# Kernel optimization log

Measured on AMD Instinct MI355X. Metric: run time of the kernel, lower is better.

## Reference

```python
import jax, jax.numpy as jnp
import numpy as np

B, S, D, E, F = 2, 2048, 1024, 8, 4096


def setup_inputs() -> dict:
    key = jax.random.key(0)
    k1, k2, k3, k4 = jax.random.split(key, 4)
    x = jax.random.normal(k1, (B, S, D), dtype=jnp.float32)
    gate_w = jax.random.normal(k2, (E, D), dtype=jnp.float32) * 0.02
    w1 = jax.random.normal(k3, (E, D, F), dtype=jnp.float32) * 0.02
    w2 = jax.random.normal(k4, (E, F, D), dtype=jnp.float32) * 0.02
    return {"x": x, "gate_w": gate_w, "w1": w1, "w2": w2}


def reference(x, gate_w, w1, w2):
    b, s, d = x.shape
    n_experts = w1.shape[0]
    tokens = x.reshape(-1, d)                      # (T, D)
    logits = tokens @ gate_w.T                     # (T, E) router (Linear, no bias)
    expert_ids = jnp.argmax(logits, axis=-1)       # top-1 routing (T,)
    dispatch = jax.nn.one_hot(expert_ids, n_experts, dtype=tokens.dtype)  # (T, E)
    # dense all-experts reference of the grouped GEMM: h_e = tokens @ w1[e]
    h = jnp.einsum('td,edf->etf', tokens, w1)      # (E, T, F)
    h = jax.nn.gelu(h, approximate=False)          # torch F.gelu default = exact erf
    out_e = jnp.einsum('etf,efd->etd', h, w2)      # (E, T, D)
    # scatter back: each token takes exactly its assigned expert's output
    out = jnp.einsum('etd,te->td', out_e, dispatch)
    return out.reshape(b, s, d)
```

## Files before the change

kernel.cpp:

```cpp
#include <hip/hip_runtime.h>
#include <hip/hip_bf16.h>
#include <math.h>

#define T_TOK 4096
#define D_DIM 1024
#define E_EXP 8
#define F_DIM 4096
#define BM 128
#define BN 128
#define BK 32
#define LDK 40
#define MAX_TILES 40

typedef __attribute__((ext_vector_type(8))) short short8;
typedef __attribute__((ext_vector_type(4))) float float4v;

__device__ __forceinline__ short f2b(float f) {
    union { float f; unsigned u; } v; v.f = f;
    unsigned r = v.u + 0x7fffu + ((v.u >> 16) & 1u);
    return (short)(r >> 16);
}

__global__ void router_kernel(const float* __restrict__ x, const float* __restrict__ gw,
                              int* __restrict__ eid, int* __restrict__ rnk,
                              int* __restrict__ counts) {
    int lane = threadIdx.x & 63;
    int wave = threadIdx.x >> 6;
    int t = blockIdx.x * 4 + wave;
    const float* xr = x + (size_t)t * D_DIM;
    float p[E_EXP];
#pragma unroll
    for (int e = 0; e < E_EXP; ++e) p[e] = 0.f;
#pragma unroll
    for (int i = 0; i < D_DIM / 64; ++i) {
        float v = xr[lane + 64 * i];
#pragma unroll
        for (int e = 0; e < E_EXP; ++e)
            p[e] = fmaf(v, gw[e * D_DIM + lane + 64 * i], p[e]);
    }
#pragma unroll
    for (int off = 32; off > 0; off >>= 1) {
#pragma unroll
        for (int e = 0; e < E_EXP; ++e) p[e] += __shfl_down(p[e], off, 64);
    }
    if (lane == 0) {
        int best = 0; float bv = p[0];
#pragma unroll
        for (int e = 1; e < E_EXP; ++e) if (p[e] > bv) { bv = p[e]; best = e; }
        eid[t] = best;
        rnk[t] = atomicAdd(&counts[best], 1);
    }
}

__global__ void prefix_kernel(const int* __restrict__ counts, int* __restrict__ offsets,
                              int* __restrict__ tmap) {
    int off = 0;
    offsets[0] = 0;
    int nt = 0;
    for (int e = 0; e < E_EXP; ++e) {
        int c = counts[e];
        for (int m0 = 0; m0 < c; m0 += BM) {
            tmap[nt * 3 + 0] = e;
            tmap[nt * 3 + 1] = off + m0;
            tmap[nt * 3 + 2] = (c - m0 < BM) ? (c - m0) : BM;
            ++nt;
        }
        off += c;
        offsets[e + 1] = off;
    }
    for (; nt < MAX_TILES; ++nt) tmap[nt * 3 + 2] = 0;
}

__global__ void scatter_kernel(const int* __restrict__ eid, const int* __restrict__ rnk,
                               const int* __restrict__ offsets, int* __restrict__ sorted) {
    int t = blockIdx.x * 256 + threadIdx.x;
    sorted[offsets[eid[t]] + rnk[t]] = t;
}

__global__ __launch_bounds__(256) void gemm1_kernel(const float* __restrict__ x,
                                                    const float* __restrict__ w1,
                                                    const int* __restrict__ sorted,
                                                    const int* __restrict__ tmap,
                                                    short* __restrict__ hbuf) {
    __shared__ short As[BM * LDK];
    __shared__ short Bs[BN * LDK];
    __shared__ int srow[BM];
    int mt = blockIdx.y;
    int m_count = tmap[mt * 3 + 2];
    if (m_count == 0) return;
    int e = tmap[mt * 3 + 0];
    int row0 = tmap[mt * 3 + 1];
    int n0 = blockIdx.x * BN;
    int tid = threadIdx.x;
    if (tid < BM) srow[tid] = sorted[row0 + (tid < m_count ? tid : m_count - 1)];
    __syncthreads();

    int lane = tid & 63, wave = tid >> 6;
    int wm = (wave & 1) * 64, wn = (wave >> 1) * 64;
    float4v acc[4][4];
#pragma unroll
    for (int i = 0; i < 4; ++i)
#pragma unroll
        for (int j = 0; j < 4; ++j) acc[i][j] = (float4v)(0.f);

    int ar = tid >> 1;
    int ac = (tid & 1) * 16;
    int bn = tid & 127;
    int bq = (tid >> 7) * 16;
    const float* abase = x + (size_t)srow[ar] * D_DIM + ac;
    const float* bbase = w1 + (size_t)e * D_DIM * F_DIM + (size_t)bq * F_DIM + (n0 + bn);

    for (int k0 = 0; k0 < D_DIM; k0 += BK) {
        {
            const float* ap = abase + k0;
            float4v f0 = *(const float4v*)(ap);
            float4v f1 = *(const float4v*)(ap + 4);
            float4v f2 = *(const float4v*)(ap + 8);
            float4v f3 = *(const float4v*)(ap + 12);
            short8 s0, s1;
#pragma unroll
            for (int c = 0; c < 4; ++c) {
                s0[c] = f2b(f0[c]); s0[4 + c] = f2b(f1[c]);
                s1[c] = f2b(f2[c]); s1[4 + c] = f2b(f3[c]);
            }
            *(short8*)(&As[ar * LDK + ac]) = s0;
            *(short8*)(&As[ar * LDK + ac + 8]) = s1;
        }
        {
            const float* bp = bbase + (size_t)k0 * F_DIM;
            float v[16];
#pragma unroll
            for (int j = 0; j < 16; ++j) v[j] = bp[(size_t)j * F_DIM];
            short8 s0, s1;
#pragma unroll
            for (int j = 0; j < 8; ++j) { s0[j] = f2b(v[j]); s1[j] = f2b(v[8 + j]); }
            *(short8*)(&Bs[bn * LDK + bq]) = s0;
            *(short8*)(&Bs[bn * LDK + bq + 8]) = s1;
        }
        __syncthreads();
        short8 af[4], bf[4];
#pragma unroll
        for (int i = 0; i < 4; ++i)
            af[i] = *(const short8*)(&As[(wm + i * 16 + (lane & 15)) * LDK + (lane >> 4) * 8]);
#pragma unroll
        for (int j = 0; j < 4; ++j)
            bf[j] = *(const short8*)(&Bs[(wn + j * 16 + (lane & 15)) * LDK + (lane >> 4) * 8]);
#pragma unroll
        for (int i = 0; i < 4; ++i)
#pragma unroll
            for (int j = 0; j < 4; ++j)
                acc[i][j] = __builtin_amdgcn_mfma_f32_16x16x32_bf16(af[i], bf[j], acc[i][j], 0, 0, 0);
        __syncthreads();
    }
    int rbase = (lane >> 4) * 4;
    int cbase = lane & 15;
#pragma unroll
    for (int i = 0; i < 4; ++i) {
#pragma unroll
        for (int r = 0; r < 4; ++r) {
            int row = wm + i * 16 + rbase + r;
            if (row < m_count) {
                short* hp = hbuf + (size_t)(row0 + row) * F_DIM + n0 + wn + cbase;
#pragma unroll
                for (int j = 0; j < 4; ++j) {
                    float s = acc[i][j][r];
                    float g = 0.5f * s * (1.f + erff(s * 0.70710678118f));
                    hp[j * 16] = f2b(g);
                }
            }
        }
    }
}

__global__ __launch_bounds__(256) void gemm2_kernel(const short* __restrict__ hbuf,
                                                    const float* __restrict__ w2,
                                                    const int* __restrict__ sorted,
                                                    const int* __restrict__ tmap,
                                                    float* __restrict__ out) {
    __shared__ short As[BM * LDK];
    __shared__ short Bs[BN * LDK];
    __shared__ int srow[BM];
    int mt = blockIdx.y;
    int m_count = tmap[mt * 3 + 2];
    if (m_count == 0) return;
    int e = tmap[mt * 3 + 0];
    int row0 = tmap[mt * 3 + 1];
    int n0 = blockIdx.x * BN;
    int tid = threadIdx.x;
    if (tid < BM) srow[tid] = sorted[row0 + (tid < m_count ? tid : m_count - 1)];
    __syncthreads();

    int lane = tid & 63, wave = tid >> 6;
    int wm = (wave & 1) * 64, wn = (wave >> 1) * 64;
    float4v acc[4][4];
#pragma unroll
    for (int i = 0; i < 4; ++i)
#pragma unroll
        for (int j = 0; j < 4; ++j) acc[i][j] = (float4v)(0.f);

    int ar = tid >> 1;
    int ac = (tid & 1) * 16;
    int bn = tid & 127;
    int bq = (tid >> 7) * 16;
    int arc = ar < m_count ? ar : m_count - 1;
    const short* abase = hbuf + (size_t)(row0 + arc) * F_DIM + ac;
    const float* bbase = w2 + (size_t)e * F_DIM * D_DIM + (size_t)bq * D_DIM + (n0 + bn);

    for (int k0 = 0; k0 < F_DIM; k0 += BK) {
        {
            const short* ap = abase + k0;
            *(short8*)(&As[ar * LDK + ac]) = *(const short8*)(ap);
            *(short8*)(&As[ar * LDK + ac + 8]) = *(const short8*)(ap + 8);
        }
        {
            const float* bp = bbase + (size_t)k0 * D_DIM;
            float v[16];
#pragma unroll
            for (int j = 0; j < 16; ++j) v[j] = bp[(size_t)j * D_DIM];
            short8 s0, s1;
#pragma unroll
            for (int j = 0; j < 8; ++j) { s0[j] = f2b(v[j]); s1[j] = f2b(v[8 + j]); }
            *(short8*)(&Bs[bn * LDK + bq]) = s0;
            *(short8*)(&Bs[bn * LDK + bq + 8]) = s1;
        }
        __syncthreads();
        short8 af[4], bf[4];
#pragma unroll
        for (int i = 0; i < 4; ++i)
            af[i] = *(const short8*)(&As[(wm + i * 16 + (lane & 15)) * LDK + (lane >> 4) * 8]);
#pragma unroll
        for (int j = 0; j < 4; ++j)
            bf[j] = *(const short8*)(&Bs[(wn + j * 16 + (lane & 15)) * LDK + (lane >> 4) * 8]);
#pragma unroll
        for (int i = 0; i < 4; ++i)
#pragma unroll
            for (int j = 0; j < 4; ++j)
                acc[i][j] = __builtin_amdgcn_mfma_f32_16x16x32_bf16(af[i], bf[j], acc[i][j], 0, 0, 0);
        __syncthreads();
    }
    int rbase = (lane >> 4) * 4;
    int cbase = lane & 15;
#pragma unroll
    for (int i = 0; i < 4; ++i) {
#pragma unroll
        for (int r = 0; r < 4; ++r) {
            int row = wm + i * 16 + rbase + r;
            if (row < m_count) {
                float* op = out + (size_t)srow[row] * D_DIM + n0 + wn + cbase;
#pragma unroll
                for (int j = 0; j < 4; ++j) op[j * 16] = acc[i][j][r];
            }
        }
    }
}

extern "C" void kernel_launch(void* const* d_in, const int* in_sizes, int n_in,
                              void* d_out, int out_size, void* d_ws, size_t ws_size,
                              hipStream_t stream) {
    const float* x  = (const float*)d_in[0];
    const float* gw = (const float*)d_in[1];
    const float* w1 = (const float*)d_in[2];
    const float* w2 = (const float*)d_in[3];
    float* out = (float*)d_out;
    char* ws = (char*)d_ws;

    int* counts  = (int*)(ws);
    int* offsets = (int*)(ws + 64);
    int* tmap    = (int*)(ws + 128);
    int* eid     = (int*)(ws + 1024);
    int* rnk     = (int*)(ws + 17408);
    int* sorted  = (int*)(ws + 33792);
    short* hbuf  = (short*)(ws + 51200);

    hipMemsetAsync(counts, 0, 32, stream);
    router_kernel<<<T_TOK / 4, 256, 0, stream>>>(x, gw, eid, rnk, counts);
    prefix_kernel<<<1, 1, 0, stream>>>(counts, offsets, tmap);
    scatter_kernel<<<T_TOK / 256, 256, 0, stream>>>(eid, rnk, offsets, sorted);
    gemm1_kernel<<<dim3(F_DIM / BN, MAX_TILES), 256, 0, stream>>>(x, w1, sorted, tmap, hbuf);
    gemm2_kernel<<<dim3(D_DIM / BN, MAX_TILES), 256, 0, stream>>>(hbuf, w2, sorted, tmap, out);
}
```

Baseline: 555.4 us.

## Pre-convert inputs and transposed weights to bf16, split-K gemm2 with atomics

Adds kernels that convert x to bf16 and transpose-convert w1/w2 into K-contiguous bf16 layouts in workspace, so the GEMMs can load operands with plain vector loads instead of converting fp32 inside the main loop. gemm2 is split along F into four K-slices that accumulate into a zeroed output with atomicAdd, raising the number of blocks. The weight conversion runs on every call and moves all 256MB of fp32 weights, which may outweigh the savings. Atomics also make the fp32 summation order nondeterministic.

```diff
diff --git a/kernel.cpp b/kernel.cpp
--- a/kernel.cpp
+++ b/kernel.cpp
@@ -1,5 +1,4 @@
 #include <hip/hip_runtime.h>
-#include <hip/hip_bf16.h>
 #include <math.h>
 
 #define T_TOK 4096
@@ -11,6 +10,7 @@
 #define BK 32
 #define LDK 40
 #define MAX_TILES 40
+#define KSPLIT 4
 
 typedef __attribute__((ext_vector_type(8))) short short8;
 typedef __attribute__((ext_vector_type(4))) float float4v;
@@ -75,6 +75,189 @@
                                const int* __restrict__ offsets, int* __restrict__ sorted) {
     int t = blockIdx.x * 256 + threadIdx.x;
     sorted[offsets[eid[t]] + rnk[t]] = t;
+}
+
+__global__ __launch_bounds__(256) void cvt_x_kernel(const float* __restrict__ x,
+                                                    short* __restrict__ xb) {
+    size_t base = ((size_t)blockIdx.x * 256 + threadIdx.x) * 16;
+    float4v f0 = *(const float4v*)(x + base);
+    float4v f1 = *(const float4v*)(x + base + 4);
+    float4v f2 = *(const float4v*)(x + base + 8);
+    float4v f3 = *(const float4v*)(x + base + 12);
+    short8 s0, s1;
+#pragma unroll
+    for (int c = 0; c < 4; ++c) {
+        s0[c] = f2b(f0[c]); s0[4 + c] = f2b(f1[c]);
+        s1[c] = f2b(f2[c]); s1[4 + c] = f2b(f3[c]);
+    }
+    *(short8*)(xb + base) = s0;
+    *(short8*)(xb + base + 8) = s1;
+}
+
+__global__ __launch_bounds__(256) void tconv_kernel(const float* __restrict__ in,
+                                                    short* __restrict__ outp, int R, int C) {
+    __shared__ short t[64][72];
+    size_t slab = (size_t)R * C;
+    const float* ip = in + (size_t)blockIdx.z * slab + (size_t)(blockIdx.y * 64) * C + blockIdx.x * 64;
+    short* op = outp + (size_t)blockIdx.z * slab + (size_t)(blockIdx.x * 64) * R + blockIdx.y * 64;
+    int tid = threadIdx.x;
+    int r = tid >> 2, c4 = (tid & 3) * 16;
+    const float* p = ip + (size_t)r * C + c4;
+    float4v f0 = *(const float4v*)(p);
+    float4v f1 = *(const float4v*)(p + 4);
+    float4v f2 = *(const float4v*)(p + 8);
+    float4v f3 = *(const float4v*)(p + 12);
+#pragma unroll
+    for (int j = 0; j < 4; ++j) {
+        t[c4 + j][r]      = f2b(f0[j]);
+        t[c4 + 4 + j][r]  = f2b(f1[j]);
+        t[c4 + 8 + j][r]  = f2b(f2[j]);
+        t[c4 + 12 + j][r] = f2b(f3[j]);
+    }
+    __syncthreads();
+    short* q = op + (size_t)r * R + c4;
+    *(short8*)q       = *(const short8*)&t[r][c4];
+    *(short8*)(q + 8) = *(const short8*)&t[r][c4 + 8];
+}
+
+__global__ __launch_bounds__(256) void gemm1_bf16(const short* __restrict__ xb,
+                                                  const short* __restrict__ w1b,
+                                                  const int* __restrict__ sorted,
+                                                  const int* __restrict__ tmap,
+                                                  short* __restrict__ hbuf) {
+    __shared__ short As[BM * LDK];
+    __shared__ short Bs[BN * LDK];
+    __shared__ int srow[BM];
+    int mt = blockIdx.y;
+    int m_count = tmap[mt * 3 + 2];
+    if (m_count == 0) return;
+    int e = tmap[mt * 3 + 0];
+    int row0 = tmap[mt * 3 + 1];
+    int n0 = blockIdx.x * BN;
+    int tid = threadIdx.x;
+    if (tid < BM) srow[tid] = sorted[row0 + (tid < m_count ? tid : m_count - 1)];
+    __syncthreads();
+
+    int lane = tid & 63, wave = tid >> 6;
+    int wm = (wave & 1) * 64, wn = (wave >> 1) * 64;
+    float4v acc[4][4];
+#pragma unroll
+    for (int i = 0; i < 4; ++i)
+#pragma unroll
+        for (int j = 0; j < 4; ++j) acc[i][j] = (float4v)(0.f);
+
+    int r2 = tid >> 1;
+    int c2 = (tid & 1) * 16;
+    const short* abase = xb + (size_t)srow[r2] * D_DIM + c2;
+    const short* bbase = w1b + (size_t)e * D_DIM * F_DIM + (size_t)(n0 + r2) * D_DIM + c2;
+
+    for (int k0 = 0; k0 < D_DIM; k0 += BK) {
+        *(short8*)(&As[r2 * LDK + c2])     = *(const short8*)(abase + k0);
+        *(short8*)(&As[r2 * LDK + c2 + 8]) = *(const short8*)(abase + k0 + 8);
+        *(short8*)(&Bs[r2 * LDK + c2])     = *(const short8*)(bbase + k0);
+        *(short8*)(&Bs[r2 * LDK + c2 + 8]) = *(const short8*)(bbase + k0 + 8);
+        __syncthreads();
+        short8 af[4], bf[4];
+#pragma unroll
+        for (int i = 0; i < 4; ++i)
+            af[i] = *(const short8*)(&As[(wm + i * 16 + (lane & 15)) * LDK + (lane >> 4) * 8]);
+#pragma unroll
+        for (int j = 0; j < 4; ++j)
+            bf[j] = *(const short8*)(&Bs[(wn + j * 16 + (lane & 15)) * LDK + (lane >> 4) * 8]);
+#pragma unroll
+        for (int i = 0; i < 4; ++i)
+#pragma unroll
+            for (int j = 0; j < 4; ++j)
+                acc[i][j] = __builtin_amdgcn_mfma_f32_16x16x32_bf16(af[i], bf[j], acc[i][j], 0, 0, 0);
+        __syncthreads();
+    }
+    int rbase = (lane >> 4) * 4;
+    int cbase = lane & 15;
+#pragma unroll
+    for (int i = 0; i < 4; ++i) {
+#pragma unroll
+        for (int r = 0; r < 4; ++r) {
+            int row = wm + i * 16 + rbase + r;
+            if (row < m_count) {
+                short* hp = hbuf + (size_t)(row0 + row) * F_DIM + n0 + wn + cbase;
+#pragma unroll
+                for (int j = 0; j < 4; ++j) {
+                    float s = acc[i][j][r];
+                    float g = 0.5f * s * (1.f + erff(s * 0.70710678118f));
+                    hp[j * 16] = f2b(g);
+                }
+            }
+        }
+    }
+}
+
+__global__ __launch_bounds__(256) void gemm2_bf16(const short* __restrict__ hbuf,
+                                                  const short* __restrict__ w2b,
+                                                  const int* __restrict__ sorted,
+                                                  const int* __restrict__ tmap,
+                                                  float* __restrict__ out) {
+    __shared__ short As[BM * LDK];
+    __shared__ short Bs[BN * LDK];
+    __shared__ int srow[BM];
+    int mt = blockIdx.y;
+    int m_count = tmap[mt * 3 + 2];
+    if (m_count == 0) return;
+    int e = tmap[mt * 3 + 0];
+    int row0 = tmap[mt * 3 + 1];
+    int n0 = blockIdx.x * BN;
+    int ks0 = blockIdx.z * (F_DIM / KSPLIT);
+    int tid = threadIdx.x;
+    if (tid < BM) srow[tid] = sorted[row0 + (tid < m_count ? tid : m_count - 1)];
+    __syncthreads();
+
+    int lane = tid & 63, wave = tid >> 6;
+    int wm = (wave & 1) * 64, wn = (wave >> 1) * 64;
+    float4v acc[4][4];
+#pragma unroll
+    for (int i = 0; i < 4; ++i)
+#pragma unroll
+        for (int j = 0; j < 4; ++j) acc[i][j] = (float4v)(0.f);
+
+    int r2 = tid >> 1;
+    int c2 = (tid & 1) * 16;
+    int arc = r2 < m_count ? r2 : m_count - 1;
+    const short* abase = hbuf + (size_t)(row0 + arc) * F_DIM + c2 + ks0;
+    const short* bbase = w2b + (size_t)e * F_DIM * D_DIM + (size_t)(n0 + r2) * F_DIM + c2 + ks0;
+
+    for (int k0 = 0; k0 < F_DIM / KSPLIT; k0 += BK) {
+        *(short8*)(&As[r2 * LDK + c2])     = *(const short8*)(abase + k0);
+        *(short8*)(&As[r2 * LDK + c2 + 8]) = *(const short8*)(abase + k0 + 8);
+        *(short8*)(&Bs[r2 * LDK + c2])     = *(const short8*)(bbase + k0);
+        *(short8*)(&Bs[r2 * LDK + c2 + 8]) = *(const short8*)(bbase + k0 + 8);
+        __syncthreads();
+        short8 af[4], bf[4];
+#pragma unroll
+        for (int i = 0; i < 4; ++i)
+            af[i] = *(const short8*)(&As[(wm + i * 16 + (lane & 15)) * LDK + (lane >> 4) * 8]);
+#pragma unroll
+        for (int j = 0; j < 4; ++j)
+            bf[j] = *(const short8*)(&Bs[(wn + j * 16 + (lane & 15)) * LDK + (lane >> 4) * 8]);
+#pragma unroll
+        for (int i = 0; i < 4; ++i)
+#pragma unroll
+            for (int j = 0; j < 4; ++j)
+                acc[i][j] = __builtin_amdgcn_mfma_f32_16x16x32_bf16(af[i], bf[j], acc[i][j], 0, 0, 0);
+        __syncthreads();
+    }
+    int rbase = (lane >> 4) * 4;
+    int cbase = lane & 15;
+#pragma unroll
+    for (int i = 0; i < 4; ++i) {
+#pragma unroll
+        for (int r = 0; r < 4; ++r) {
+            int row = wm + i * 16 + rbase + r;
+            if (row < m_count) {
+                float* op = out + (size_t)srow[row] * D_DIM + n0 + wn + cbase;
+#pragma unroll
+                for (int j = 0; j < 4; ++j) atomicAdd(op + j * 16, acc[i][j][r]);
+            }
+        }
+    }
 }
 
 __global__ __launch_bounds__(256) void gemm1_kernel(const float* __restrict__ x,
@@ -272,10 +455,33 @@
     int* sorted  = (int*)(ws + 33792);
     short* hbuf  = (short*)(ws + 51200);
 
+    const size_t HB  = 33554432ull;
+    const size_t XB  = 8388608ull;
+    const size_t WB  = 67108864ull;
+    short* xb  = (short*)(ws + 51200 + HB);
+    short* w1b = (short*)(ws + 51200 + HB + XB);
+    short* w2b = (short*)(ws + 51200 + HB + XB + WB);
+    const size_t need = 51200ull + HB + XB + 2ull * WB;
+    bool fast = ws_size >= need;
+
     hipMemsetAsync(counts, 0, 32, stream);
     router_kernel<<<T_TOK / 4, 256, 0, stream>>>(x, gw, eid, rnk, counts);
+
+    if (fast) {
+        hipMemsetAsync(out, 0, (size_t)T_TOK * D_DIM * 4, stream);
+        cvt_x_kernel<<<T_TOK * D_DIM / (256 * 16), 256, 0, stream>>>(x, xb);
+        tconv_kernel<<<dim3(F_DIM / 64, D_DIM / 64, E_EXP), 256, 0, stream>>>(w1, w1b, D_DIM, F_DIM);
+        tconv_kernel<<<dim3(D_DIM / 64, F_DIM / 64, E_EXP), 256, 0, stream>>>(w2, w2b, F_DIM, D_DIM);
+    }
+
     prefix_kernel<<<1, 1, 0, stream>>>(counts, offsets, tmap);
     scatter_kernel<<<T_TOK / 256, 256, 0, stream>>>(eid, rnk, offsets, sorted);
-    gemm1_kernel<<<dim3(F_DIM / BN, MAX_TILES), 256, 0, stream>>>(x, w1, sorted, tmap, hbuf);
-    gemm2_kernel<<<dim3(D_DIM / BN, MAX_TILES), 256, 0, stream>>>(hbuf, w2, sorted, tmap, out);
-}
+
+    if (fast) {
+        gemm1_bf16<<<dim3(F_DIM / BN, MAX_TILES), 256, 0, stream>>>(xb, w1b, sorted, tmap, hbuf);
+        gemm2_bf16<<<dim3(D_DIM / BN, MAX_TILES, KSPLIT), 256, 0, stream>>>(hbuf, w2b, sorted, tmap, out);
+    } else {
+        gemm1_kernel<<<dim3(F_DIM / BN, MAX_TILES), 256, 0, stream>>>(x, w1, sorted, tmap, hbuf);
+        gemm2_kernel<<<dim3(D_DIM / BN, MAX_TILES), 256, 0, stream>>>(hbuf, w2, sorted, tmap, out);
+    }
+}
```

Result: slower. 570.0 us (+2.6%).
